# Performance work log

Hardware: AMD Instinct MI355X
Metric: run time of the kernel (lower is better)

Reference implementation:

```python
import jax, jax.numpy as jnp
import numpy as np

B, S, E, H = 4, 2048, 2048, 16
D = E // H  # head_dim = 128
MAX_LEN = 2048


def _make_freqs():
    # standard RoPE frequencies: theta = 10000^{-2i/D}
    inv_freq = 1.0 / (10000.0 ** (np.arange(0, D, 2, dtype=np.float32) / D))  # [D/2]
    t = np.arange(MAX_LEN, dtype=np.float32)
    ang = np.outer(t, inv_freq)  # [max_len, D/2]
    cos = ang.reshape(1, MAX_LEN, 1, D // 2)
    return jnp.asarray(np.cos(cos)), jnp.asarray(np.sin(cos))


def setup_inputs() -> dict:
    key = jax.random.key(0)
    ks = jax.random.split(key, 10)
    sc = 1.0 / np.sqrt(E)
    freqs_cos, freqs_sin = _make_freqs()
    return {
        "x": jax.random.normal(ks[0], (B, S, E), dtype=jnp.float32),
        "freqs_cos": freqs_cos,
        "freqs_sin": freqs_sin,
        "wq": jax.random.normal(ks[1], (E, E), dtype=jnp.float32) * sc,
        "bq": jax.random.normal(ks[2], (E,), dtype=jnp.float32) * 0.01,
        "wk": jax.random.normal(ks[3], (E, E), dtype=jnp.float32) * sc,
        "bk": jax.random.normal(ks[4], (E,), dtype=jnp.float32) * 0.01,
        "wv": jax.random.normal(ks[5], (E, E), dtype=jnp.float32) * sc,
        "bv": jax.random.normal(ks[6], (E,), dtype=jnp.float32) * 0.01,
        "wo": jax.random.normal(ks[7], (E, E), dtype=jnp.float32) * sc,
        "bo": jax.random.normal(ks[8], (E,), dtype=jnp.float32) * 0.01,
    }


def _rope(t, cos, sin):
    # t: [B, S, H, D]; complex multiply on interleaved (even, odd) pairs
    tr = t.reshape(*t.shape[:-1], -1, 2)  # [B,S,H,D/2,2]
    xr, xi = tr[..., 0], tr[..., 1]
    rr = xr * cos - xi * sin
    ri = xr * sin + xi * cos
    return jnp.stack([rr, ri], axis=-1).reshape(t.shape)


def reference(x, freqs_cos, freqs_sin, wq, bq, wk, bk, wv, bv, wo, bo):
    b, s, _ = x.shape
    q = (x @ wq.T + bq).reshape(b, s, H, D)
    k = (x @ wk.T + bk).reshape(b, s, H, D)
    v = (x @ wv.T + bv).reshape(b, s, H, D)
    cos, sin = freqs_cos[:, :s], freqs_sin[:, :s]
    q = _rope(q, cos, sin)
    k = _rope(k, cos, sin)
    # FAITHFUL to source: q,k,v stay [B,S,H,D], so matmul contracts over D
    # producing per-position head-head scores [B,S,H,H] (no transpose to BHSD).
    qk = jnp.einsum("bshd,bsgd->bshg", q, k) / jnp.sqrt(jnp.float32(D))
    att = jax.nn.softmax(qk, axis=-1)
    att_out = jnp.einsum("bshg,bsgd->bshd", att, v)  # [B,S,H,D]
    # torch: transpose(1,2).contiguous().view(B,S,-1) -> h-major flatten
    att_out = jnp.transpose(att_out, (0, 2, 1, 3)).reshape(b, s, -1)
    return att_out @ wo.T + bo
```

## Files before the change

### kernel.cpp

```cpp
#include <hip/hip_runtime.h>
#include <stdint.h>

typedef unsigned short u16t;
typedef __attribute__((ext_vector_type(8))) short frag8;
typedef __attribute__((ext_vector_type(4))) float facc4;

#define S_LEN 2048
#define E_DIM 2048

__device__ __forceinline__ u16t f2bf(float f) {
    union { float f; uint32_t u; } c; c.f = f;
    return (u16t)((c.u + 0x7fffu + ((c.u >> 16) & 1u)) >> 16);
}

__global__ __launch_bounds__(256) void cvt_kernel(const float* __restrict__ src,
                                                  u16t* __restrict__ dst, int n4) {
    int i = blockIdx.x * 256 + threadIdx.x;
    if (i >= n4) return;
    float4 v = ((const float4*)src)[i];
    ushort4 o;
    o.x = f2bf(v.x); o.y = f2bf(v.y); o.z = f2bf(v.z); o.w = f2bf(v.w);
    ((ushort4*)dst)[i] = o;
}

struct CvtPtrs { const float* s[4]; u16t* d[4]; };
__global__ __launch_bounds__(256) void cvt4_kernel(CvtPtrs p, int n4) {
    int i = blockIdx.x * 256 + threadIdx.x;
    if (i >= n4) return;
    const int w = blockIdx.y;
    float4 v = ((const float4*)p.s[w])[i];
    ushort4 o;
    o.x = f2bf(v.x); o.y = f2bf(v.y); o.z = f2bf(v.z); o.w = f2bf(v.w);
    ((ushort4*)p.d[w])[i] = o;
}

__device__ __forceinline__ void gldl16(const u16t* g, u16t* l) {
    __builtin_amdgcn_global_load_lds(
        (__attribute__((address_space(1))) void*)(g),
        (__attribute__((address_space(3))) void*)(l), 16, 0, 0);
}

__device__ __forceinline__ void gemm_core(const u16t* __restrict__ A,
                                          const u16t* __restrict__ Bw,
                                          u16t* As, u16t* Bs,
                                          facc4 acc[4][8]) {
    const int t    = threadIdx.x;
    const int lane = t & 63;
    const int wid  = t >> 6;
    const int m16  = lane & 15;
    const int quad = lane >> 4;
    const int sw   = (m16 >> 1) & 3;
    const int wm   = (wid & 1) * 64;
    const int wn   = (wid >> 1) * 128;
    const size_t bm0 = (size_t)blockIdx.y * 128;
    const size_t bn0 = (size_t)blockIdx.x * 256;

#pragma unroll
    for (int i = 0; i < 4; ++i)
#pragma unroll
        for (int j = 0; j < 8; ++j) acc[i][j] = facc4{0.f, 0.f, 0.f, 0.f};

    const u16t* Ab = A + bm0 * E_DIM;
    const u16t* Bb = Bw + bn0 * E_DIM;

    const int l8 = lane * 8;
    const int rA0 = (wid * 1024 + l8) >> 5;
    const int rA1 = rA0 + 16;
    const int rB0 = (wid * 2048 + l8) >> 5;
    const int rB1 = rB0 + 16, rB2 = rB0 + 32, rB3 = rB0 + 48;
    const int c3 = lane & 3;
    const size_t gA0 = (size_t)rA0 * E_DIM + ((c3 ^ ((rA0 >> 1) & 3)) * 8);
    const size_t gA1 = (size_t)rA1 * E_DIM + ((c3 ^ ((rA1 >> 1) & 3)) * 8);
    const size_t gB0 = (size_t)rB0 * E_DIM + ((c3 ^ ((rB0 >> 1) & 3)) * 8);
    const size_t gB1 = (size_t)rB1 * E_DIM + ((c3 ^ ((rB1 >> 1) & 3)) * 8);
    const size_t gB2 = (size_t)rB2 * E_DIM + ((c3 ^ ((rB2 >> 1) & 3)) * 8);
    const size_t gB3 = (size_t)rB3 * E_DIM + ((c3 ^ ((rB3 >> 1) & 3)) * 8);
    u16t* lA = As + wid * 1024;
    u16t* lB = Bs + wid * 2048;

    for (int k0 = 0; k0 < E_DIM; k0 += 32) {
        __syncthreads();
        gldl16(Ab + gA0 + k0, lA);
        gldl16(Ab + gA1 + k0, lA + 512);
        gldl16(Bb + gB0 + k0, lB);
        gldl16(Bb + gB1 + k0, lB + 512);
        gldl16(Bb + gB2 + k0, lB + 1024);
        gldl16(Bb + gB3 + k0, lB + 1536);
        __syncthreads();

        frag8 av[4], bv[8];
#pragma unroll
        for (int i = 0; i < 4; ++i)
            av[i] = *(const frag8*)(As + (wm + i * 16 + m16) * 32 + (quad ^ sw) * 8);
#pragma unroll
        for (int j = 0; j < 8; ++j)
            bv[j] = *(const frag8*)(Bs + (wn + j * 16 + m16) * 32 + (quad ^ sw) * 8);
#pragma unroll
        for (int i = 0; i < 4; ++i)
#pragma unroll
            for (int j = 0; j < 8; ++j)
                acc[i][j] = __builtin_amdgcn_mfma_f32_16x16x32_bf16(
                    av[i], bv[j], acc[i][j], 0, 0, 0);
    }
}

struct QkvArgs {
    const u16t* w[3];
    const float* bias[3];
    u16t* out[3];
};

__global__ __launch_bounds__(256, 2)
void qkv_gemm(const u16t* __restrict__ xb, QkvArgs args,
              const float* __restrict__ fcos, const float* __restrict__ fsin) {
    __shared__ u16t As[128 * 32];
    __shared__ u16t Bs[256 * 32];
    facc4 acc[4][8];
    const int z = blockIdx.z;
    gemm_core(xb, args.w[z], As, Bs, acc);

    const int t    = threadIdx.x;
    const int lane = t & 63;
    const int m16  = lane & 15;
    const int quad = lane >> 4;
    const int wid  = t >> 6;
    const int wm   = (wid & 1) * 64;
    const int wn   = (wid >> 1) * 128;
    const int bm0  = blockIdx.y * 128;
    const int bn0  = blockIdx.x * 256;
    const bool rope = (z < 2);
    u16t* out = args.out[z];
    const float* bias = args.bias[z];

#pragma unroll
    for (int i = 0; i < 4; ++i) {
#pragma unroll
        for (int j = 0; j < 8; ++j) {
            const int n = bn0 + wn + j * 16 + m16;
            const float bn_ = bias[n];
#pragma unroll
            for (int r = 0; r < 4; ++r) {
                const int m = bm0 + wm + i * 16 + quad * 4 + r;
                float v = acc[i][j][r] + bn_;
                const float part = __shfl_xor(v, 1, 64);
                if (rope) {
                    const int s = m & (S_LEN - 1);
                    const int p = (n & 127) >> 1;
                    const float cs = fcos[s * 64 + p];
                    const float sn = fsin[s * 64 + p];
                    v = (n & 1) ? (part * sn + v * cs) : (v * cs - part * sn);
                }
                out[(size_t)m * E_DIM + n] = f2bf(v);
            }
        }
    }
}

__global__ __launch_bounds__(256, 2)
void out_gemm(const u16t* __restrict__ sh, const u16t* __restrict__ wob,
              const float* __restrict__ bo, float* __restrict__ out) {
    __shared__ u16t As[128 * 32];
    __shared__ u16t Bs[256 * 32];
    facc4 acc[4][8];
    gemm_core(sh, wob, As, Bs, acc);

    const int t    = threadIdx.x;
    const int lane = t & 63;
    const int m16  = lane & 15;
    const int quad = lane >> 4;
    const int wid  = t >> 6;
    const int wm   = (wid & 1) * 64;
    const int wn   = (wid >> 1) * 128;
    const int bm0  = blockIdx.y * 128;
    const int bn0  = blockIdx.x * 256;

#pragma unroll
    for (int i = 0; i < 4; ++i) {
#pragma unroll
        for (int j = 0; j < 8; ++j) {
            const int n = bn0 + wn + j * 16 + m16;
            const float bn_ = bo[n];
#pragma unroll
            for (int r = 0; r < 4; ++r) {
                const int m = bm0 + wm + i * 16 + quad * 4 + r;
                out[(size_t)m * E_DIM + n] = acc[i][j][r] + bn_;
            }
        }
    }
}

__global__ __launch_bounds__(256)
void attn_kernel(const u16t* __restrict__ qb, const u16t* __restrict__ kb,
                 const u16t* __restrict__ vb, u16t* __restrict__ sh) {
    __shared__ u16t Vs[4][16 * 136];
    __shared__ u16t Pt[4][16 * 32];

    const int t    = threadIdx.x;
    const int wid  = t >> 6;
    const int lane = t & 63;
    const int m16  = lane & 15;
    const int quad = lane >> 4;
    const int tk   = blockIdx.x * 4 + wid;
    const int b    = tk >> 11;
    const int s    = tk & (S_LEN - 1);
    const size_t row = (size_t)tk * E_DIM;

    frag8 aq[4], ak[4];
    const u16t* qrow = qb + row + m16 * 128 + quad * 8;
    const u16t* krow = kb + row + m16 * 128 + quad * 8;
#pragma unroll
    for (int ks = 0; ks < 4; ++ks) {
        aq[ks] = *(const frag8*)(qrow + ks * 32);
        ak[ks] = *(const frag8*)(krow + ks * 32);
    }

    u16t* vs = Vs[wid];
#pragma unroll
    for (int c = 0; c < 4; ++c) {
        const int e  = c * 512 + lane * 8;
        const int vr = e >> 7, vc = e & 127;
        *(uint4*)(vs + vr * 136 + vc) = *(const uint4*)(vb + row + e);
    }

    facc4 sacc = facc4{0.f, 0.f, 0.f, 0.f};
#pragma unroll
    for (int ks = 0; ks < 4; ++ks)
        sacc = __builtin_amdgcn_mfma_f32_16x16x32_bf16(aq[ks], ak[ks], sacc, 0, 0, 0);

    float p[4], mx[4], sm[4];
#pragma unroll
    for (int r = 0; r < 4; ++r) { p[r] = sacc[r] * 0.08838834764831845f; mx[r] = p[r]; }
#pragma unroll
    for (int msk = 1; msk < 16; msk <<= 1)
#pragma unroll
        for (int r = 0; r < 4; ++r) mx[r] = fmaxf(mx[r], __shfl_xor(mx[r], msk, 64));
#pragma unroll
    for (int r = 0; r < 4; ++r) { p[r] = __expf(p[r] - mx[r]); sm[r] = p[r]; }
#pragma unroll
    for (int msk = 1; msk < 16; msk <<= 1)
#pragma unroll
        for (int r = 0; r < 4; ++r) sm[r] += __shfl_xor(sm[r], msk, 64);

    u16t* pt = Pt[wid];
#pragma unroll
    for (int r = 0; r < 4; ++r)
        pt[(quad * 4 + r) * 32 + m16] = f2bf(p[r] / sm[r]);
    *(uint2*)(pt + m16 * 32 + 16 + quad * 4) = uint2{0u, 0u};

    __builtin_amdgcn_wave_barrier();

    const frag8 aP = *(const frag8*)(pt + m16 * 32 + quad * 8);

    facc4 oacc[8];
#pragma unroll
    for (int d = 0; d < 8; ++d) oacc[d] = facc4{0.f, 0.f, 0.f, 0.f};
#pragma unroll
    for (int dblk = 0; dblk < 8; ++dblk) {
        union { u16t u[8]; frag8 f; } bb;
#pragma unroll
        for (int j = 0; j < 8; ++j)
            bb.u[j] = vs[((quad * 8 + j) & 15) * 136 + dblk * 16 + m16];
        oacc[dblk] = __builtin_amdgcn_mfma_f32_16x16x32_bf16(aP, bb.f, oacc[dblk], 0, 0, 0);
    }

    __builtin_amdgcn_wave_barrier();
#pragma unroll
    for (int dblk = 0; dblk < 8; ++dblk)
#pragma unroll
        for (int r = 0; r < 4; ++r)
            vs[(quad * 4 + r) * 136 + dblk * 16 + m16] = f2bf(oacc[dblk][r]);
    __builtin_amdgcn_wave_barrier();

    const size_t base = ((size_t)b << 22) + (size_t)(s >> 4) * E_DIM
                      + (size_t)((s & 15) * 128);
#pragma unroll
    for (int hb = 0; hb < 4; ++hb) {
        const int h = hb * 4 + quad;
        const uint4 ov = *(const uint4*)(vs + h * 136 + m16 * 8);
        *(uint4*)(sh + base + ((size_t)h << 18) + m16 * 8) = ov;
    }
}

extern "C" void kernel_launch(void* const* d_in, const int* in_sizes, int n_in,
                              void* d_out, int out_size, void* d_ws, size_t ws_size,
                              hipStream_t stream) {
    const float* x    = (const float*)d_in[0];
    const float* fcos = (const float*)d_in[1];
    const float* fsin = (const float*)d_in[2];
    const float* wq   = (const float*)d_in[3];
    const float* bq   = (const float*)d_in[4];
    const float* wk   = (const float*)d_in[5];
    const float* bk   = (const float*)d_in[6];
    const float* wv   = (const float*)d_in[7];
    const float* bv   = (const float*)d_in[8];
    const float* wo   = (const float*)d_in[9];
    const float* bo   = (const float*)d_in[10];
    float* out = (float*)d_out;

    char* ws = (char*)d_ws;
    u16t* xb  = (u16t*)(ws);
    u16t* qb  = (u16t*)(ws + 33554432ull);
    u16t* kb  = (u16t*)(ws + 67108864ull);
    u16t* vb  = (u16t*)(ws + 100663296ull);
    u16t* wqb = (u16t*)(ws + 134217728ull);
    u16t* wkb = (u16t*)(ws + 142606336ull);
    u16t* wvb = (u16t*)(ws + 150994944ull);
    u16t* wob = (u16t*)(ws + 159383552ull);

    cvt_kernel<<<16384, 256, 0, stream>>>(x, xb, 4194304);
    CvtPtrs cp;
    cp.s[0] = wq; cp.s[1] = wk; cp.s[2] = wv; cp.s[3] = wo;
    cp.d[0] = wqb; cp.d[1] = wkb; cp.d[2] = wvb; cp.d[3] = wob;
    cvt4_kernel<<<dim3(4096, 4), 256, 0, stream>>>(cp, 1048576);

    QkvArgs qa;
    qa.w[0] = wqb; qa.w[1] = wkb; qa.w[2] = wvb;
    qa.bias[0] = bq; qa.bias[1] = bk; qa.bias[2] = bv;
    qa.out[0] = qb; qa.out[1] = kb; qa.out[2] = vb;
    qkv_gemm<<<dim3(8, 64, 3), 256, 0, stream>>>(xb, qa, fcos, fsin);

    attn_kernel<<<2048, 256, 0, stream>>>(qb, kb, vb, xb);

    out_gemm<<<dim3(8, 64), 256, 0, stream>>>(xb, wob, bo, out);
}
```

Baseline: 539.9 us.

## Enlarge GEMM tiles to 256x256 and double-buffer LDS loads

The shared GEMM core moves from 128x256 to 256x256 block tiles, with 128x128 per wave, so each loaded tile feeds more MFMAs. It also double-buffers the LDS staging: the next k-slice is loaded while the current one is computed, leaving one barrier per iteration instead of two. Grids are halved to match, and launch bounds drop to one block per CU because each thread now holds 256 accumulator floats. This cuts occupancy and wave count (768 and 256 blocks), which could hurt latency hiding and load balance.

After: 772.9 us. +43.2%, slower.

```diff
diff --git a/kernel.cpp b/kernel.cpp
--- a/kernel.cpp
+++ b/kernel.cpp
@@ -43,60 +43,64 @@
 __device__ __forceinline__ void gemm_core(const u16t* __restrict__ A,
                                           const u16t* __restrict__ Bw,
                                           u16t* As, u16t* Bs,
-                                          facc4 acc[4][8]) {
+                                          facc4 acc[8][8]) {
     const int t    = threadIdx.x;
     const int lane = t & 63;
     const int wid  = t >> 6;
     const int m16  = lane & 15;
     const int quad = lane >> 4;
     const int sw   = (m16 >> 1) & 3;
-    const int wm   = (wid & 1) * 64;
+    const int wm   = (wid & 1) * 128;
     const int wn   = (wid >> 1) * 128;
-    const size_t bm0 = (size_t)blockIdx.y * 128;
+    const size_t bm0 = (size_t)blockIdx.y * 256;
     const size_t bn0 = (size_t)blockIdx.x * 256;
 
 #pragma unroll
-    for (int i = 0; i < 4; ++i)
+    for (int i = 0; i < 8; ++i)
 #pragma unroll
         for (int j = 0; j < 8; ++j) acc[i][j] = facc4{0.f, 0.f, 0.f, 0.f};
 
     const u16t* Ab = A + bm0 * E_DIM;
     const u16t* Bb = Bw + bn0 * E_DIM;
 
-    const int l8 = lane * 8;
-    const int rA0 = (wid * 1024 + l8) >> 5;
-    const int rA1 = rA0 + 16;
-    const int rB0 = (wid * 2048 + l8) >> 5;
-    const int rB1 = rB0 + 16, rB2 = rB0 + 32, rB3 = rB0 + 48;
     const int c3 = lane & 3;
-    const size_t gA0 = (size_t)rA0 * E_DIM + ((c3 ^ ((rA0 >> 1) & 3)) * 8);
-    const size_t gA1 = (size_t)rA1 * E_DIM + ((c3 ^ ((rA1 >> 1) & 3)) * 8);
-    const size_t gB0 = (size_t)rB0 * E_DIM + ((c3 ^ ((rB0 >> 1) & 3)) * 8);
-    const size_t gB1 = (size_t)rB1 * E_DIM + ((c3 ^ ((rB1 >> 1) & 3)) * 8);
-    const size_t gB2 = (size_t)rB2 * E_DIM + ((c3 ^ ((rB2 >> 1) & 3)) * 8);
-    const size_t gB3 = (size_t)rB3 * E_DIM + ((c3 ^ ((rB3 >> 1) & 3)) * 8);
-    u16t* lA = As + wid * 1024;
-    u16t* lB = Bs + wid * 2048;
-
-    for (int k0 = 0; k0 < E_DIM; k0 += 32) {
+    size_t g_[4];
+#pragma unroll
+    for (int c = 0; c < 4; ++c) {
+        const int r = wid * 64 + c * 16 + (lane >> 2);
+        g_[c] = (size_t)r * E_DIM + ((c3 ^ ((r >> 1) & 3)) * 8);
+    }
+    u16t* la = As + wid * 2048;
+    u16t* lb = Bs + wid * 2048;
+
+#pragma unroll
+    for (int c = 0; c < 4; ++c) gldl16(Ab + g_[c], la + c * 512);
+#pragma unroll
+    for (int c = 0; c < 4; ++c) gldl16(Bb + g_[c], lb + c * 512);
+
+    for (int kk = 0; kk < 64; ++kk) {
+        const int cur = kk & 1;
         __syncthreads();
-        gldl16(Ab + gA0 + k0, lA);
-        gldl16(Ab + gA1 + k0, lA + 512);
-        gldl16(Bb + gB0 + k0, lB);
-        gldl16(Bb + gB1 + k0, lB + 512);
-        gldl16(Bb + gB2 + k0, lB + 1024);
-        gldl16(Bb + gB3 + k0, lB + 1536);
-        __syncthreads();
-
-        frag8 av[4], bv[8];
-#pragma unroll
-        for (int i = 0; i < 4; ++i)
-            av[i] = *(const frag8*)(As + (wm + i * 16 + m16) * 32 + (quad ^ sw) * 8);
+        if (kk < 63) {
+            const int k1 = (kk + 1) * 32;
+            u16t* na = la + (cur ^ 1) * 8192;
+            u16t* nb = lb + (cur ^ 1) * 8192;
+#pragma unroll
+            for (int c = 0; c < 4; ++c) gldl16(Ab + g_[c] + k1, na + c * 512);
+#pragma unroll
+            for (int c = 0; c < 4; ++c) gldl16(Bb + g_[c] + k1, nb + c * 512);
+        }
+        const u16t* Ah = As + cur * 8192;
+        const u16t* Bh = Bs + cur * 8192;
+        frag8 av[8], bv[8];
+#pragma unroll
+        for (int i = 0; i < 8; ++i)
+            av[i] = *(const frag8*)(Ah + (wm + i * 16 + m16) * 32 + (quad ^ sw) * 8);
 #pragma unroll
         for (int j = 0; j < 8; ++j)
-            bv[j] = *(const frag8*)(Bs + (wn + j * 16 + m16) * 32 + (quad ^ sw) * 8);
-#pragma unroll
-        for (int i = 0; i < 4; ++i)
+            bv[j] = *(const frag8*)(Bh + (wn + j * 16 + m16) * 32 + (quad ^ sw) * 8);
+#pragma unroll
+        for (int i = 0; i < 8; ++i)
 #pragma unroll
             for (int j = 0; j < 8; ++j)
                 acc[i][j] = __builtin_amdgcn_mfma_f32_16x16x32_bf16(
@@ -110,12 +114,12 @@
     u16t* out[3];
 };
 
-__global__ __launch_bounds__(256, 2)
+__global__ __launch_bounds__(256, 1)
 void qkv_gemm(const u16t* __restrict__ xb, QkvArgs args,
               const float* __restrict__ fcos, const float* __restrict__ fsin) {
-    __shared__ u16t As[128 * 32];
-    __shared__ u16t Bs[256 * 32];
-    facc4 acc[4][8];
+    __shared__ u16t As[2 * 256 * 32];
+    __shared__ u16t Bs[2 * 256 * 32];
+    facc4 acc[8][8];
     const int z = blockIdx.z;
     gemm_core(xb, args.w[z], As, Bs, acc);
 
@@ -124,16 +128,16 @@
     const int m16  = lane & 15;
     const int quad = lane >> 4;
     const int wid  = t >> 6;
-    const int wm   = (wid & 1) * 64;
+    const int wm   = (wid & 1) * 128;
     const int wn   = (wid >> 1) * 128;
-    const int bm0  = blockIdx.y * 128;
+    const int bm0  = blockIdx.y * 256;
     const int bn0  = blockIdx.x * 256;
     const bool rope = (z < 2);
     u16t* out = args.out[z];
     const float* bias = args.bias[z];
 
 #pragma unroll
-    for (int i = 0; i < 4; ++i) {
+    for (int i = 0; i < 8; ++i) {
 #pragma unroll
         for (int j = 0; j < 8; ++j) {
             const int n = bn0 + wn + j * 16 + m16;
@@ -156,12 +160,12 @@
     }
 }
 
-__global__ __launch_bounds__(256, 2)
+__global__ __launch_bounds__(256, 1)
 void out_gemm(const u16t* __restrict__ sh, const u16t* __restrict__ wob,
               const float* __restrict__ bo, float* __restrict__ out) {
-    __shared__ u16t As[128 * 32];
-    __shared__ u16t Bs[256 * 32];
-    facc4 acc[4][8];
+    __shared__ u16t As[2 * 256 * 32];
+    __shared__ u16t Bs[2 * 256 * 32];
+    facc4 acc[8][8];
     gemm_core(sh, wob, As, Bs, acc);
 
     const int t    = threadIdx.x;
@@ -169,13 +173,13 @@
     const int m16  = lane & 15;
     const int quad = lane >> 4;
     const int wid  = t >> 6;
-    const int wm   = (wid & 1) * 64;
+    const int wm   = (wid & 1) * 128;
     const int wn   = (wid >> 1) * 128;
-    const int bm0  = blockIdx.y * 128;
+    const int bm0  = blockIdx.y * 256;
     const int bn0  = blockIdx.x * 256;
 
 #pragma unroll
-    for (int i = 0; i < 4; ++i) {
+    for (int i = 0; i < 8; ++i) {
 #pragma unroll
         for (int j = 0; j < 8; ++j) {
             const int n = bn0 + wn + j * 16 + m16;
@@ -317,9 +321,9 @@
     qa.w[0] = wqb; qa.w[1] = wkb; qa.w[2] = wvb;
     qa.bias[0] = bq; qa.bias[1] = bk; qa.bias[2] = bv;
     qa.out[0] = qb; qa.out[1] = kb; qa.out[2] = vb;
-    qkv_gemm<<<dim3(8, 64, 3), 256, 0, stream>>>(xb, qa, fcos, fsin);
+    qkv_gemm<<<dim3(8, 32, 3), 256, 0, stream>>>(xb, qa, fcos, fsin);
 
     attn_kernel<<<2048, 256, 0, stream>>>(qb, kb, vb, xb);
 
-    out_gemm<<<dim3(8, 64), 256, 0, stream>>>(xb, wob, bo, out);
-}
+    out_gemm<<<dim3(8, 32), 256, 0, stream>>>(xb, wob, bo, out);
+}
```
